# Kernel tuning notes

Measured on AMD Instinct MI355X. Metric: run time of the kernel, lower is better.

The kernel has to match this reference:

```python
import jax, jax.numpy as jnp
import numpy as np

B, L_TOT, C = 64, 8192, 4
WIN = 16
H = 64
NL = 8
GROUPS = 8          # head groups
SA_GROUP = 4        # SortAttn group (hard-coded default)
GH = H * 2 // SA_GROUP   # 32
SEG = 4
CLS = 4
IN_SIZE = C * WIN   # 64 == H (all layers share input dim)


def _shuffle(x):
    # torch Shuffle: transpose(-1,-2).contiguous().view(original_shape)
    return jnp.swapaxes(x, -1, -2).reshape(x.shape)


def setup_inputs() -> dict:
    key = jax.random.key(0)
    ks = jax.random.split(key, 32)
    s = 0.1
    f32 = jnp.float32
    return {
        "x": jax.random.normal(ks[0], (B, L_TOT, C), f32),
        "h0_param": jnp.zeros((NL, 1, H), f32),
        "gru_w_ih": (jax.random.normal(ks[1], (NL, 3 * H, IN_SIZE), f32) * s),
        "gru_w_hh": (jax.random.normal(ks[2], (NL, 3 * H, H), f32) * s),
        "gru_b_ih": (jax.random.normal(ks[3], (NL, 3 * H), f32) * s),
        "gru_b_hh": (jax.random.normal(ks[4], (NL, 3 * H), f32) * s),
        "attn_w1": (jax.random.normal(ks[5], (NL, H, H), f32) * s),
        "attn_w2": (jax.random.normal(ks[6], (NL, GH, GH), f32) * s),
        "attn_w3": (jax.random.normal(ks[7], (NL, GH, GH), f32) * s),
        "attn_w4": (jax.random.normal(ks[8], (NL, H, 2 * H), f32) * s),
        "seg_w1": (jax.random.normal(ks[9], (SEG, H // GROUPS), f32) * s),
        "seg_b1": (jax.random.normal(ks[10], (SEG,), f32) * s),
        "seg_w2": (jax.random.normal(ks[11], (SEG, SEG), f32) * s),
        "seg_b2": (jax.random.normal(ks[12], (SEG,), f32) * s),
        "seg_w3": (jax.random.normal(ks[13], (SEG, SEG), f32) * s),
        "seg_b3": (jax.random.normal(ks[14], (SEG,), f32) * s),
        "seg_w4": (jax.random.normal(ks[15], (WIN, GROUPS), f32) * s),
        "seg_b4": (jax.random.normal(ks[16], (WIN,), f32) * s),
        "cls_w1": (jax.random.normal(ks[17], (CLS, H // GROUPS), f32) * s),
        "cls_b1": (jax.random.normal(ks[18], (CLS,), f32) * s),
        "cls_w2": (jax.random.normal(ks[19], (CLS, CLS), f32) * s),
        "cls_b2": (jax.random.normal(ks[20], (CLS,), f32) * s),
        "cls_w3": (jax.random.normal(ks[21], (CLS, CLS), f32) * s),
        "cls_b3": (jax.random.normal(ks[22], (CLS,), f32) * s),
        "cls_w4": (jax.random.normal(ks[23], (CLS, CLS * GROUPS), f32) * s),
        "cls_b4": (jax.random.normal(ks[24], (CLS,), f32) * s),
    }


def reference(x, h0_param, gru_w_ih, gru_w_hh, gru_b_ih, gru_b_hh,
              attn_w1, attn_w2, attn_w3, attn_w4,
              seg_w1, seg_b1, seg_w2, seg_b2, seg_w3, seg_b3, seg_w4, seg_b4,
              cls_w1, cls_b1, cls_w2, cls_b2, cls_w3, cls_b3, cls_w4, cls_b4):
    b, l, c = x.shape
    lw = l // WIN
    xs = x.reshape(b, lw, WIN * c)                     # (b, lw, IN_SIZE)
    h0 = jnp.broadcast_to(h0_param, (NL, b, H))        # hidden_0 * ones(1,b,1)

    def gru_cell(inp, h, w_ih, w_hh, b_ih, b_hh):
        gi = inp @ w_ih.T + b_ih                       # (b, 3H)
        gh = h @ w_hh.T + b_hh
        i_r, i_z, i_n = jnp.split(gi, 3, axis=1)
        h_r, h_z, h_n = jnp.split(gh, 3, axis=1)
        r = jax.nn.sigmoid(i_r + h_r)
        z = jax.nn.sigmoid(i_z + h_z)
        n = jnp.tanh(i_n + r * h_n)
        return (1.0 - z) * n + z * h

    def sort_attn(h, w1, w2, w3, w4):
        se = jnp.stack([h, jnp.sort(h, axis=1)], axis=1)   # (b, 2, H)
        a = se @ w1.T                                       # (b, 2, H)
        a = a.reshape(b, SA_GROUP, GH)                      # Flatten+Unflatten
        a = _shuffle(a) @ w2.T
        a = jax.nn.relu(_shuffle(a) @ w3.T)
        scores = jax.nn.sigmoid(a.reshape(b, SA_GROUP * GH) @ w4.T)  # (b, H)
        return h * scores

    def step(hidden, xt):
        inp = xt
        new = []
        for i in range(NL):
            hi = gru_cell(inp, hidden[i], gru_w_ih[i], gru_w_hh[i], gru_b_ih[i], gru_b_hh[i])
            hi = sort_attn(hi, attn_w1[i], attn_w2[i], attn_w3[i], attn_w4[i])
            new.append(hi)
            inp = hi
        return jnp.stack(new, axis=0), inp

    h_final, outs = jax.lax.scan(step, h0, jnp.swapaxes(xs, 0, 1))
    ys = jnp.swapaxes(outs, 0, 1)                      # (b, lw, H)

    # ---- seg head ----
    t = ys.reshape(b, lw, GROUPS, H // GROUPS)         # (b, lw, 8, 8)
    t = t @ seg_w1.T + seg_b1                          # (b, lw, 8, 4)
    t = _shuffle(t) @ seg_w2.T + seg_b2
    t = _shuffle(t) @ seg_w3.T + seg_b3
    t = t.reshape(b, lw, SEG, GROUPS)                  # Flatten(2)+Unflatten
    t = t @ seg_w4.T + seg_b4
    seg = jnp.swapaxes(t, -1, -2).reshape(b, lw * WIN, SEG)  # (b, l, 4)

    # ---- avg_pool1d(k=11, s=1) with 10 zero history frames ----
    pool_in = jnp.concatenate([jnp.zeros((b, 10, SEG), seg.dtype), seg], axis=1)
    cs = jnp.concatenate([jnp.zeros((b, 1, SEG), seg.dtype),
                          jnp.cumsum(pool_in, axis=1)], axis=1)
    pool_seg = (cs[:, 11:] - cs[:, :-11]) / 11.0       # (b, l, 4)

    # ---- cls head ----
    u = ys.reshape(b * lw, GROUPS, H // GROUPS)
    u = u @ cls_w1.T + cls_b1
    u = _shuffle(u) @ cls_w2.T + cls_b2
    u = jax.nn.relu(_shuffle(u) @ cls_w3.T + cls_b3)
    cls = u.reshape(b * lw, CLS * GROUPS) @ cls_w4.T + cls_b4
    cls = cls.reshape(b, lw, CLS).mean(axis=1)         # (b, 4)

    return (pool_seg, cls, ys, h_final, seg)
```

## Files before the change

kernel.cpp:

```cpp
#include <hip/hip_runtime.h>
#include <math.h>

#define LW  512

typedef unsigned short u16;
typedef float f32x4 __attribute__((ext_vector_type(4)));
typedef u16 u16x4 __attribute__((ext_vector_type(4)));
typedef u16 u16x8 __attribute__((ext_vector_type(8)));
typedef unsigned u32x2v __attribute__((ext_vector_type(2)));
typedef __bf16 bf16x8 __attribute__((ext_vector_type(8)));

__device__ __forceinline__ u16 f2bf(float f) {
    return __builtin_bit_cast(u16, (__bf16)f);
}
__device__ __forceinline__ float bf2f(u16 h) {
    unsigned u = ((unsigned)h) << 16;
    return __builtin_bit_cast(float, u);
}
__device__ __forceinline__ float sigm(float x) {
    return __builtin_amdgcn_rcpf(1.0f + __expf(-x));
}
__device__ __forceinline__ float tanhfast(float x) {
    return 1.0f - 2.0f * __builtin_amdgcn_rcpf(1.0f + __expf(2.0f * x));
}
__device__ __forceinline__ f32x4 mfma16(u16x8 a, u16x8 b, f32x4 c) {
    return __builtin_amdgcn_mfma_f32_16x16x32_bf16(
        __builtin_bit_cast(bf16x8, a), __builtin_bit_cast(bf16x8, b), c, 0, 0, 0);
}
__device__ __forceinline__ unsigned ld_sys(const unsigned* p) {
    return __hip_atomic_load(p, __ATOMIC_RELAXED, __HIP_MEMORY_SCOPE_SYSTEM);
}
__device__ __forceinline__ void st_sys(unsigned* p, unsigned v) {
    __hip_atomic_store(p, v, __ATOMIC_RELAXED, __HIP_MEMORY_SCOPE_SYSTEM);
}
__device__ __forceinline__ void poll_ge(const unsigned* p, unsigned want) {
    while (ld_sys(p) < want) __builtin_amdgcn_s_sleep(2);
    asm volatile("" ::: "memory");
    __builtin_amdgcn_sched_barrier(0);
}
__device__ __forceinline__ void poll4(const unsigned* p, unsigned want) {
    for (;;) {
        unsigned m0 = ld_sys(p + 0), m1 = ld_sys(p + 1);
        unsigned m2 = ld_sys(p + 2), m3 = ld_sys(p + 3);
        unsigned a = m0 < m1 ? m0 : m1;
        unsigned b = m2 < m3 ? m2 : m3;
        if ((a < b ? a : b) >= want) break;
        __builtin_amdgcn_s_sleep(2);
    }
    asm volatile("" ::: "memory");
    __builtin_amdgcn_sched_barrier(0);
}
__device__ __forceinline__ void bar_lgkm() {
    asm volatile("s_waitcnt lgkmcnt(0)" ::: "memory");
    __builtin_amdgcn_s_barrier();
}

template<int CTRL> __device__ __forceinline__ float dppf(float v) {
    return __builtin_bit_cast(float,
        __builtin_amdgcn_mov_dpp(__builtin_bit_cast(int, v), CTRL, 0xF, 0xF, false));
}
template<int OFF> __device__ __forceinline__ float swzf(float v) {
    return __builtin_bit_cast(float,
        __builtin_amdgcn_ds_swizzle(__builtin_bit_cast(int, v), OFF));
}
template<int J> __device__ __forceinline__ float xch(float v) {
    if constexpr (J == 1)  return dppf<0xB1>(v);
    else if constexpr (J == 2)  return dppf<0x4E>(v);
    else if constexpr (J == 4)  return dppf<0x141>(dppf<0x1B>(v));
    else if constexpr (J == 8)  return dppf<0x140>(dppf<0x141>(v));
    else if constexpr (J == 16) return swzf<0x401F>(v);
    else return __shfl_xor(v, 32);
}
#define STG4(KK, J) { \
    float o0 = xch<J>(v0), o1 = xch<J>(v1), o2 = xch<J>(v2), o3 = xch<J>(v3); \
    bool k = (((ln & KK) == 0) == ((ln & J) == 0)); \
    v0 = k ? fminf(v0, o0) : fmaxf(v0, o0); \
    v1 = k ? fminf(v1, o1) : fmaxf(v1, o1); \
    v2 = k ? fminf(v2, o2) : fmaxf(v2, o2); \
    v3 = k ? fminf(v3, o3) : fmaxf(v3, o3); }

__global__ __launch_bounds__(256) void init_flags(unsigned* f) {
    f[blockIdx.x * 256 + threadIdx.x] = 0u;
}

__global__ __launch_bounds__(128) void prep_A(
    const float* __restrict__ aw1, const float* __restrict__ aw2,
    const float* __restrict__ aw3, u16* __restrict__ Abf)
{
    const int l   = blockIdx.x;
    const int tid = threadIdx.x;
    __shared__ float T1[128][65];
    __shared__ float T2[128][65];
    for (int ch = 0; ch < 2; ++ch) {
        for (int i = tid; i < 128 * 64; i += 128) {
            int f = i >> 6, j = i & 63;
            int s = ch * 64 + j;
            T1[f][j] = ((f >> 6) == (s >> 6))
                       ? aw1[l * 4096 + (f & 63) * 64 + (s & 63)] : 0.f;
        }
        __syncthreads();
        for (int i = tid; i < 128 * 64; i += 128) {
            int gg = i >> 6, j = i & 63;
            int n = gg & 31, r = gg >> 5;
            float acc = 0.f;
            #pragma unroll 8
            for (int k = 0; k < 32; ++k) {
                int g = r * 32 + k;
                int src = (g & 3) * 32 + (g >> 2);
                acc += aw2[l * 1024 + n * 32 + k] * T1[src][j];
            }
            T2[gg][j] = acc;
        }
        __syncthreads();
        for (int i = tid; i < 128 * 64; i += 128) {
            int ff = i >> 6, j = i & 63;
            int n = ff & 31, r = ff >> 5;
            float acc = 0.f;
            #pragma unroll 8
            for (int k = 0; k < 32; ++k) {
                int g = r * 32 + k;
                int src = (g & 3) * 32 + (g >> 2);
                acc += aw3[l * 1024 + n * 32 + k] * T2[src][j];
            }
            Abf[((size_t)l * 128 + ff) * 128 + ch * 64 + j] = f2bf(acc);
        }
        __syncthreads();
    }
}

__global__ __launch_bounds__(256, 1) void rnn_kernel(
    const float* __restrict__ x, const float* __restrict__ h0,
    const float* __restrict__ w_ih, const float* __restrict__ w_hh,
    const float* __restrict__ bih, const float* __restrict__ bhh,
    const u16* __restrict__ Abf, const float* __restrict__ aw4,
    float* __restrict__ ys, float* __restrict__ hfin,
    unsigned* __restrict__ flags, unsigned* __restrict__ ring32, int D)
{
    const int l   = blockIdx.x >> 3;
    const int g   = blockIdx.x & 7;
    const int bb0 = g * 8;
    const int tid = threadIdx.x;
    const int w   = tid >> 6;
    const int ln  = tid & 63;
    const int l15 = ln & 15;
    const int l4  = ln >> 4;
    const bool bp = (D < LW);

    unsigned* myflag = flags + (size_t)(l * 8 + g) * 32;
    unsigned* pflag  = flags + (size_t)((l - 1) * 8 + g) * 32;
    unsigned* myccnt = flags + 4096 + (size_t)(l * 8 + g) * 32;
    unsigned* nccnt  = flags + 4096 + (size_t)((l + 1) * 8 + g) * 32;

    __shared__ __align__(16) u16 Hin[2][16][72];
    __shared__ __align__(16) u16 hbf[16][72];
    __shared__ __align__(16) u16 seF[16][136];
    __shared__ __align__(16) u16 w4A[16][136];

    for (int i = tid; i < 16 * 72; i += 256) {
        int r = i / 72, c = i % 72;
        if (r >= 8) { Hin[0][r][c] = 0; Hin[1][r][c] = 0; hbf[r][c] = 0; }
    }
    for (int i = tid; i < 16 * 136; i += 256) {
        int r = i / 136;
        if (r >= 8) { w4A[r][i % 136] = 0; seF[r][i % 136] = 0; }
    }

    const int o = 16 * w + l15;
    auto ldw8 = [](const float* p) {
        float4 v0 = *(const float4*)p;
        float4 v1 = *(const float4*)(p + 4);
        u16x8 r;
        r[0] = f2bf(v0.x); r[1] = f2bf(v0.y); r[2] = f2bf(v0.z); r[3] = f2bf(v0.w);
        r[4] = f2bf(v1.x); r[5] = f2bf(v1.y); r[6] = f2bf(v1.z); r[7] = f2bf(v1.w);
        return r;
    };
    const float* ih = w_ih + l * 12288;
    const float* hh = w_hh + l * 12288;
    u16x8 Br[4], Bz[4], Bni[2], Bnh[2], B4f[4], BA[2][4];
    Br[0] = ldw8(ih + o * 64 + l4 * 8);        Br[1] = ldw8(ih + o * 64 + 32 + l4 * 8);
    Br[2] = ldw8(hh + o * 64 + l4 * 8);        Br[3] = ldw8(hh + o * 64 + 32 + l4 * 8);
    Bz[0] = ldw8(ih + (64 + o) * 64 + l4 * 8); Bz[1] = ldw8(ih + (64 + o) * 64 + 32 + l4 * 8);
    Bz[2] = ldw8(hh + (64 + o) * 64 + l4 * 8); Bz[3] = ldw8(hh + (64 + o) * 64 + 32 + l4 * 8);
    Bni[0] = ldw8(ih + (128 + o) * 64 + l4 * 8); Bni[1] = ldw8(ih + (128 + o) * 64 + 32 + l4 * 8);
    Bnh[0] = ldw8(hh + (128 + o) * 64 + l4 * 8); Bnh[1] = ldw8(hh + (128 + o) * 64 + 32 + l4 * 8);
    #pragma unroll
    for (int kk = 0; kk < 4; ++kk)
        B4f[kk] = ldw8(aw4 + l * 8192 + o * 128 + kk * 32 + l4 * 8);
    #pragma unroll
    for (int nt = 0; nt < 2; ++nt)
        #pragma unroll
        for (int kk = 0; kk < 4; ++kk)
            BA[nt][kk] = *(const u16x8*)&Abf[((size_t)l * 128 + (16 * (2 * w + nt) + l15)) * 128
                                             + kk * 32 + l4 * 8];

    const float brs  = bih[l * 192 + o]       + bhh[l * 192 + o];
    const float bzs  = bih[l * 192 + 64 + o]  + bhh[l * 192 + 64 + o];
    const float bnis = bih[l * 192 + 128 + o];
    const float bnhs = bhh[l * 192 + 128 + o];

    float hreg[4];
    {
        float hv = h0[l * 64 + o];
        #pragma unroll
        for (int j = 0; j < 4; ++j) hreg[j] = hv;
        if (l4 < 2) {
            u16 hb = f2bf(hv);
            #pragma unroll
            for (int j = 0; j < 4; ++j) hbf[l4 * 4 + j][o] = hb;
        }
    }

    float4 stf = {0.f, 0.f, 0.f, 0.f};
    unsigned st0 = 0, st1 = 0;
    if (w >= 2) {
        const int rr = (tid - 128) >> 4, c4 = ((tid - 128) & 15) * 4;
        if (l == 0) {
            float4 a = *(const float4*)(x + (size_t)(bb0 + rr) * 32768 + c4);
            u16x4 hv;
            hv[0] = f2bf(a.x); hv[1] = f2bf(a.y); hv[2] = f2bf(a.z); hv[3] = f2bf(a.w);
            *(u16x4*)&Hin[0][rr][c4] = hv;
            stf = *(const float4*)(x + (size_t)(bb0 + rr) * 32768 + 64 + c4);
        } else {
            poll4(pflag, 1u);
            const unsigned* sp0 = ring32 + ((size_t)((l - 1) * 8 + g) * D + 0) * 256 + rr * 32 + (c4 >> 1);
            unsigned a0 = ld_sys(sp0), a1 = ld_sys(sp0 + 1);
            u32x2v dv = {a0, a1};
            *(u16x4*)&Hin[0][rr][c4] = __builtin_bit_cast(u16x4, dv);
            poll4(pflag, 2u);
            const unsigned* sp1 = ring32 + ((size_t)((l - 1) * 8 + g) * D + 1) * 256 + rr * 32 + (c4 >> 1);
            st0 = ld_sys(sp1); st1 = ld_sys(sp1 + 1);
        }
    }
    __syncthreads();

    u16x8 pAg0 = *(const u16x8*)&Hin[0][l15][l4 * 8];
    u16x8 pAg1 = *(const u16x8*)&Hin[0][l15][32 + l4 * 8];

    for (int t = 0; t < LW; ++t) {
        float hg[4];
        {
            u16x8 Ah0 = *(const u16x8*)&hbf[l15][l4 * 8];
            u16x8 Ah1 = *(const u16x8*)&hbf[l15][32 + l4 * 8];
            f32x4 z4 = {0.f, 0.f, 0.f, 0.f};
            f32x4 aR = z4, aZ = z4, aNI = z4, aNH = z4;
            aR = mfma16(pAg0, Br[0], aR);  aR = mfma16(pAg1, Br[1], aR);
            aR = mfma16(Ah0, Br[2], aR);   aR = mfma16(Ah1, Br[3], aR);
            aZ = mfma16(pAg0, Bz[0], aZ);  aZ = mfma16(pAg1, Bz[1], aZ);
            aZ = mfma16(Ah0, Bz[2], aZ);   aZ = mfma16(Ah1, Bz[3], aZ);
            aNI = mfma16(pAg0, Bni[0], aNI); aNI = mfma16(pAg1, Bni[1], aNI);
            aNH = mfma16(Ah0, Bnh[0], aNH);  aNH = mfma16(Ah1, Bnh[1], aNH);
            #pragma unroll
            for (int j = 0; j < 4; ++j) {
                float r  = sigm(aR[j] + brs);
                float zz = sigm(aZ[j] + bzs);
                float nn = tanhfast(aNI[j] + bnis + r * (aNH[j] + bnhs));
                hg[j] = (1.0f - zz) * nn + zz * hreg[j];
            }
            if (l4 < 2) {
                #pragma unroll
                for (int j = 0; j < 4; ++j) seF[l4 * 4 + j][o] = f2bf(hg[j]);
            }
        }
        bar_lgkm();

        if (l < 7) {
            asm volatile("s_waitcnt vmcnt(0)" ::: "memory");
            if (ln == 0) st_sys(myflag + w, (unsigned)t);
        }
        if (w < 2) {
            const int r0 = 4 * w;
            float v0 = bf2f(seF[r0 + 0][ln]);
            float v1 = bf2f(seF[r0 + 1][ln]);
            float v2 = bf2f(seF[r0 + 2][ln]);
            float v3 = bf2f(seF[r0 + 3][ln]);
            STG4(2, 1)
            STG4(4, 2)  STG4(4, 1)
            STG4(8, 4)  STG4(8, 2)  STG4(8, 1)
            STG4(16, 8) STG4(16, 4) STG4(16, 2) STG4(16, 1)
            STG4(32, 16) STG4(32, 8) STG4(32, 4) STG4(32, 2) STG4(32, 1)
            STG4(64, 32) STG4(64, 16) STG4(64, 8) STG4(64, 4) STG4(64, 2) STG4(64, 1)
            seF[r0 + 0][64 + ln] = f2bf(v0);
            seF[r0 + 1][64 + ln] = f2bf(v1);
            seF[r0 + 2][64 + ln] = f2bf(v2);
            seF[r0 + 3][64 + ln] = f2bf(v3);
        } else {
            const int rr = (tid - 128) >> 4, c4 = ((tid - 128) & 15) * 4;
            if (t + 1 < LW) {
                u16x4 hv;
                if (l == 0) {
                    hv[0] = f2bf(stf.x); hv[1] = f2bf(stf.y);
                    hv[2] = f2bf(stf.z); hv[3] = f2bf(stf.w);
                } else {
                    u32x2v dv = {st0, st1};
                    hv = __builtin_bit_cast(u16x4, dv);
                }
                *(u16x4*)&Hin[(t + 1) & 1][rr][c4] = hv;
            }
            if (t + 2 < LW) {
                if (l == 0) {
                    stf = *(const float4*)(x + (size_t)(bb0 + rr) * 32768 + (t + 2) * 64 + c4);
                } else {
                    poll4(pflag, (unsigned)(t + 3));
                    const unsigned* sp = ring32
                        + ((size_t)((l - 1) * 8 + g) * D + ((t + 2) & (D - 1))) * 256
                        + rr * 32 + (c4 >> 1);
                    st0 = ld_sys(sp); st1 = ld_sys(sp + 1);
                }
            }
        }
        bar_lgkm();
        if (bp && l > 0 && tid == 0)
            st_sys(myccnt, (unsigned)(t + 2));

        {
            u16x8 As0 = *(const u16x8*)&seF[l15][l4 * 8];
            u16x8 As1 = *(const u16x8*)&seF[l15][32 + l4 * 8];
            u16x8 As2 = *(const u16x8*)&seF[l15][64 + l4 * 8];
            u16x8 As3 = *(const u16x8*)&seF[l15][96 + l4 * 8];
            f32x4 z4 = {0.f, 0.f, 0.f, 0.f};
            f32x4 c0 = z4, c1 = z4;
            c0 = mfma16(As0, BA[0][0], c0); c0 = mfma16(As1, BA[0][1], c0);
            c0 = mfma16(As2, BA[0][2], c0); c0 = mfma16(As3, BA[0][3], c0);
            c1 = mfma16(As0, BA[1][0], c1); c1 = mfma16(As1, BA[1][1], c1);
            c1 = mfma16(As2, BA[1][2], c1); c1 = mfma16(As3, BA[1][3], c1);
            if (l4 < 2) {
                #pragma unroll
                for (int j = 0; j < 4; ++j) {
                    int m = l4 * 4 + j;
                    w4A[m][16 * (2 * w + 0) + l15] = f2bf(fmaxf(c0[j], 0.0f));
                    w4A[m][16 * (2 * w + 1) + l15] = f2bf(fmaxf(c1[j], 0.0f));
                }
            }
        }
        bar_lgkm();

        {
            u16x8 A40 = *(const u16x8*)&w4A[l15][l4 * 8];
            u16x8 A41 = *(const u16x8*)&w4A[l15][32 + l4 * 8];
            u16x8 A42 = *(const u16x8*)&w4A[l15][64 + l4 * 8];
            u16x8 A43 = *(const u16x8*)&w4A[l15][96 + l4 * 8];
            pAg0 = *(const u16x8*)&Hin[(t + 1) & 1][l15][l4 * 8];
            pAg1 = *(const u16x8*)&Hin[(t + 1) & 1][l15][32 + l4 * 8];
            f32x4 cs = {0.f, 0.f, 0.f, 0.f};
            cs = mfma16(A40, B4f[0], cs);
            cs = mfma16(A41, B4f[1], cs);
            cs = mfma16(A42, B4f[2], cs);
            cs = mfma16(A43, B4f[3], cs);

            if (bp && l < 7 && t >= D) {
                poll_ge(nccnt, (unsigned)(t - D + 1));
            }
            unsigned* slotp = ring32 + ((size_t)(l * 8 + g) * D + (t & (D - 1))) * 256;
            float hn[4]; u16 hb[4];
            #pragma unroll
            for (int j = 0; j < 4; ++j) {
                hn[j] = hg[j] * sigm(cs[j]);
                hreg[j] = hn[j];
                hb[j] = f2bf(hn[j]);
            }
            if (l4 < 2) {
                #pragma unroll
                for (int j = 0; j < 4; ++j) {
                    int row = l4 * 4 + j;
                    hbf[row][o] = hb[j];
                    if (l == 7) ys[(((size_t)(bb0 + row) << 9) + t) * 64 + o] = hn[j];
                    if (t == 511) hfin[((l << 6) + bb0 + row) * 64 + o] = hn[j];
                }
            }
            if (l < 7) {
                #pragma unroll
                for (int j = 0; j < 4; ++j) {
                    unsigned ob = (unsigned)__shfl_xor((int)(unsigned)hb[j], 1) & 0xffffu;
                    if (l4 < 2 && !(l15 & 1)) {
                        unsigned word = (unsigned)hb[j] | (ob << 16);
                        st_sys(&slotp[(l4 * 4 + j) * 32 + (o >> 1)], word);
                    }
                }
            }
        }
        bar_lgkm();
    }

    if (l < 7) {
        asm volatile("s_waitcnt vmcnt(0)" ::: "memory");
        if (ln == 0) st_sys(myflag + w, 512u);
    }
}

__global__ __launch_bounds__(256) void heads_kernel(
    const float* __restrict__ ys,
    const float* __restrict__ sw1, const float* __restrict__ sb1,
    const float* __restrict__ sw2, const float* __restrict__ sb2,
    const float* __restrict__ sw3, const float* __restrict__ sb3,
    const float* __restrict__ sw4, const float* __restrict__ sb4,
    const float* __restrict__ cw1, const float* __restrict__ cb1,
    const float* __restrict__ cw2, const float* __restrict__ cb2,
    const float* __restrict__ cw3, const float* __restrict__ cb3,
    const float* __restrict__ cw4, const float* __restrict__ cb4,
    float* __restrict__ seg_out, float* __restrict__ cls_tmp)
{
    const int idx = blockIdx.x * 256 + threadIdx.x;
    if (idx >= 64 * LW) return;
    const int b = idx >> 9, t = idx & 511;

    float y[64];
    const float4* yp = (const float4*)(ys + (size_t)idx * 64);
    #pragma unroll
    for (int i = 0; i < 16; ++i) {
        float4 v = yp[i];
        y[4 * i + 0] = v.x; y[4 * i + 1] = v.y; y[4 * i + 2] = v.z; y[4 * i + 3] = v.w;
    }

    float t1[8][4], t2[8][4], t3[8][4];

    #pragma unroll
    for (int g = 0; g < 8; ++g)
        #pragma unroll
        for (int s = 0; s < 4; ++s) {
            float acc = sb1[s];
            #pragma unroll
            for (int k = 0; k < 8; ++k) acc = fmaf(y[g * 8 + k], sw1[s * 8 + k], acc);
            t1[g][s] = acc;
        }
    #pragma unroll
    for (int i = 0; i < 8; ++i) {
        float sh[4];
        #pragma unroll
        for (int j = 0; j < 4; ++j) { int m = i * 4 + j; sh[j] = t1[m & 7][m >> 3]; }
        #pragma unroll
        for (int s = 0; s < 4; ++s) {
            float acc = sb2[s];
            #pragma unroll
            for (int j = 0; j < 4; ++j) acc = fmaf(sh[j], sw2[s * 4 + j], acc);
            t2[i][s] = acc;
        }
    }
    #pragma unroll
    for (int i = 0; i < 8; ++i) {
        float sh[4];
        #pragma unroll
        for (int j = 0; j < 4; ++j) { int m = i * 4 + j; sh[j] = t2[m & 7][m >> 3]; }
        #pragma unroll
        for (int s = 0; s < 4; ++s) {
            float acc = sb3[s];
            #pragma unroll
            for (int j = 0; j < 4; ++j) acc = fmaf(sh[j], sw3[s * 4 + j], acc);
            t3[i][s] = acc;
        }
    }
    #pragma unroll
    for (int w = 0; w < 16; ++w) {
        float o4[4];
        #pragma unroll
        for (int s = 0; s < 4; ++s) {
            float acc = sb4[w];
            #pragma unroll
            for (int j = 0; j < 8; ++j) {
                int f = s * 8 + j;
                acc = fmaf(t3[f >> 2][f & 3], sw4[w * 8 + j], acc);
            }
            o4[s] = acc;
        }
        float4 vv = {o4[0], o4[1], o4[2], o4[3]};
        ((float4*)seg_out)[b * 8192 + t * 16 + w] = vv;
    }

    #pragma unroll
    for (int g = 0; g < 8; ++g)
        #pragma unroll
        for (int s = 0; s < 4; ++s) {
            float acc = cb1[s];
            #pragma unroll
            for (int k = 0; k < 8; ++k) acc = fmaf(y[g * 8 + k], cw1[s * 8 + k], acc);
            t1[g][s] = acc;
        }
    #pragma unroll
    for (int i = 0; i < 8; ++i) {
        float sh[4];
        #pragma unroll
        for (int j = 0; j < 4; ++j) { int m = i * 4 + j; sh[j] = t1[m & 7][m >> 3]; }
        #pragma unroll
        for (int s = 0; s < 4; ++s) {
            float acc = cb2[s];
            #pragma unroll
            for (int j = 0; j < 4; ++j) acc = fmaf(sh[j], cw2[s * 4 + j], acc);
            t2[i][s] = acc;
        }
    }
    #pragma unroll
    for (int i = 0; i < 8; ++i) {
        float sh[4];
        #pragma unroll
        for (int j = 0; j < 4; ++j) { int m = i * 4 + j; sh[j] = t2[m & 7][m >> 3]; }
        #pragma unroll
        for (int s = 0; s < 4; ++s) {
            float acc = cb3[s];
            #pragma unroll
            for (int j = 0; j < 4; ++j) acc = fmaf(sh[j], cw3[s * 4 + j], acc);
            t3[i][s] = fmaxf(acc, 0.f);
        }
    }
    float cc[4];
    #pragma unroll
    for (int c = 0; c < 4; ++c) {
        float acc = cb4[c];
        #pragma unroll
        for (int k = 0; k < 32; ++k)
            acc = fmaf(t3[k >> 2][k & 3], cw4[c * 32 + k], acc);
        cc[c] = acc;
    }
    float4 cv = {cc[0], cc[1], cc[2], cc[3]};
    ((float4*)cls_tmp)[idx] = cv;
}

__global__ __launch_bounds__(256) void cls_reduce_kernel(
    const float* __restrict__ cls_tmp, float* __restrict__ cls_out)
{
    const int tid = threadIdx.x;
    const int b = tid >> 2, q = tid & 3;
    float ax = 0.f, ay = 0.f, az = 0.f, aw = 0.f;
    for (int t = q; t < 512; t += 4) {
        float4 v = ((const float4*)cls_tmp)[b * 512 + t];
        ax += v.x; ay += v.y; az += v.z; aw += v.w;
    }
    ax += __shfl_xor(ax, 1); ay += __shfl_xor(ay, 1);
    az += __shfl_xor(az, 1); aw += __shfl_xor(aw, 1);
    ax += __shfl_xor(ax, 2); ay += __shfl_xor(ay, 2);
    az += __shfl_xor(az, 2); aw += __shfl_xor(aw, 2);
    if (q == 0) {
        float4 rv = {ax / 512.f, ay / 512.f, az / 512.f, aw / 512.f};
        ((float4*)cls_out)[b] = rv;
    }
}

__global__ __launch_bounds__(256) void pool_kernel(
    const float* __restrict__ seg, float* __restrict__ pool_out)
{
    const int idx = blockIdx.x * 256 + threadIdx.x;
    if (idx >= 64 * 8192) return;
    const int b = idx >> 13, ll = idx & 8191;
    float ax = 0.f, ay = 0.f, az = 0.f, aw = 0.f;
    int j0 = ll - 10; if (j0 < 0) j0 = 0;
    for (int j = j0; j <= ll; ++j) {
        float4 v = ((const float4*)seg)[b * 8192 + j];
        ax += v.x; ay += v.y; az += v.z; aw += v.w;
    }
    const float inv = 1.0f / 11.0f;
    float4 ov = {ax * inv, ay * inv, az * inv, aw * inv};
    ((float4*)pool_out)[idx] = ov;
}

extern "C" void kernel_launch(void* const* d_in, const int* in_sizes, int n_in,
                              void* d_out, int out_size, void* d_ws, size_t ws_size,
                              hipStream_t stream)
{
    const float* x    = (const float*)d_in[0];
    const float* h0   = (const float*)d_in[1];
    const float* w_ih = (const float*)d_in[2];
    const float* w_hh = (const float*)d_in[3];
    const float* bihp = (const float*)d_in[4];
    const float* bhhp = (const float*)d_in[5];
    const float* aw1  = (const float*)d_in[6];
    const float* aw2  = (const float*)d_in[7];
    const float* aw3  = (const float*)d_in[8];
    const float* aw4  = (const float*)d_in[9];
    const float* sw1  = (const float*)d_in[10];
    const float* sb1  = (const float*)d_in[11];
    const float* sw2  = (const float*)d_in[12];
    const float* sb2  = (const float*)d_in[13];
    const float* sw3  = (const float*)d_in[14];
    const float* sb3  = (const float*)d_in[15];
    const float* sw4  = (const float*)d_in[16];
    const float* sb4  = (const float*)d_in[17];
    const float* cw1  = (const float*)d_in[18];
    const float* cb1  = (const float*)d_in[19];
    const float* cw2  = (const float*)d_in[20];
    const float* cb2  = (const float*)d_in[21];
    const float* cw3  = (const float*)d_in[22];
    const float* cb3  = (const float*)d_in[23];
    const float* cw4  = (const float*)d_in[24];
    const float* cb4  = (const float*)d_in[25];

    float* out      = (float*)d_out;
    float* pool_out = out;
    float* cls_out  = out + 2097152;
    float* ys_out   = out + 2097408;
    float* hfin     = out + 4194560;
    float* seg_out  = out + 4227328;
    float* cls_tmp  = pool_out;

    unsigned* flags  = (unsigned*)d_ws;
    u16*      Abf    = (u16*)((char*)d_ws + 32768);
    unsigned* ring32 = (unsigned*)((char*)d_ws + 32768 + 262144);

    size_t hdr = 32768 + 262144;
    size_t slots = (ws_size > hdr) ? (ws_size - hdr) / (56ull * 256 * 4) : 8;
    int D = 512;
    if (slots < 512) {
        D = 8;
        while ((size_t)(D * 2) <= slots && D < 512) D <<= 1;
    }

    init_flags<<<32, 256, 0, stream>>>(flags);
    prep_A<<<8, 128, 0, stream>>>(aw1, aw2, aw3, Abf);
    rnn_kernel<<<64, 256, 0, stream>>>(x, h0, w_ih, w_hh, bihp, bhhp,
                                       Abf, aw4, ys_out, hfin,
                                       flags, ring32, D);
    heads_kernel<<<128, 256, 0, stream>>>(ys_out, sw1, sb1, sw2, sb2, sw3, sb3, sw4, sb4,
                                          cw1, cb1, cw2, cb2, cw3, cb3, cw4, cb4,
                                          seg_out, cls_tmp);
    cls_reduce_kernel<<<1, 256, 0, stream>>>(cls_tmp, cls_out);
    pool_kernel<<<2048, 256, 0, stream>>>(seg_out, pool_out);
}
```

Baseline: 1.378 ms.

## Spread sort across all four waves and overlap input staging with MFMA

The bitonic sort of the eight 64-element rows was done by two waves handling four rows each while the other two waves staged the next input. Now all four waves each sort two rows, and the Hin staging, cross-layer poll and prefetch move after the MFMA issue of the next phase, so they overlap with matrix work. This shortens the critical path of the serial per-timestep sort. The trade-off is that the poll and load latency now sits inside the MFMA phase and can delay the barrier that follows.

Result: slower. 1.480 ms (+7.4%).

```diff
diff --git a/kernel.cpp b/kernel.cpp
--- a/kernel.cpp
+++ b/kernel.cpp
@@ -71,13 +71,11 @@
     else if constexpr (J == 16) return swzf<0x401F>(v);
     else return __shfl_xor(v, 32);
 }
-#define STG4(KK, J) { \
-    float o0 = xch<J>(v0), o1 = xch<J>(v1), o2 = xch<J>(v2), o3 = xch<J>(v3); \
-    bool k = (((ln & KK) == 0) == ((ln & J) == 0)); \
+#define STG2(KK, J) { \
+    float o0 = xch<J>(v0), o1 = xch<J>(v1); \
+    bool k = (((ln & KK) == 0) == (((ln) & J) == 0)); \
     v0 = k ? fminf(v0, o0) : fmaxf(v0, o0); \
-    v1 = k ? fminf(v1, o1) : fmaxf(v1, o1); \
-    v2 = k ? fminf(v2, o2) : fmaxf(v2, o2); \
-    v3 = k ? fminf(v3, o3) : fmaxf(v3, o3); }
+    v1 = k ? fminf(v1, o1) : fmaxf(v1, o1); }
 
 __global__ __launch_bounds__(256) void init_flags(unsigned* f) {
     f[blockIdx.x * 256 + threadIdx.x] = 0u;
@@ -267,46 +265,17 @@
             asm volatile("s_waitcnt vmcnt(0)" ::: "memory");
             if (ln == 0) st_sys(myflag + w, (unsigned)t);
         }
-        if (w < 2) {
-            const int r0 = 4 * w;
-            float v0 = bf2f(seF[r0 + 0][ln]);
-            float v1 = bf2f(seF[r0 + 1][ln]);
-            float v2 = bf2f(seF[r0 + 2][ln]);
-            float v3 = bf2f(seF[r0 + 3][ln]);
-            STG4(2, 1)
-            STG4(4, 2)  STG4(4, 1)
-            STG4(8, 4)  STG4(8, 2)  STG4(8, 1)
-            STG4(16, 8) STG4(16, 4) STG4(16, 2) STG4(16, 1)
-            STG4(32, 16) STG4(32, 8) STG4(32, 4) STG4(32, 2) STG4(32, 1)
-            STG4(64, 32) STG4(64, 16) STG4(64, 8) STG4(64, 4) STG4(64, 2) STG4(64, 1)
-            seF[r0 + 0][64 + ln] = f2bf(v0);
-            seF[r0 + 1][64 + ln] = f2bf(v1);
-            seF[r0 + 2][64 + ln] = f2bf(v2);
-            seF[r0 + 3][64 + ln] = f2bf(v3);
-        } else {
-            const int rr = (tid - 128) >> 4, c4 = ((tid - 128) & 15) * 4;
-            if (t + 1 < LW) {
-                u16x4 hv;
-                if (l == 0) {
-                    hv[0] = f2bf(stf.x); hv[1] = f2bf(stf.y);
-                    hv[2] = f2bf(stf.z); hv[3] = f2bf(stf.w);
-                } else {
-                    u32x2v dv = {st0, st1};
-                    hv = __builtin_bit_cast(u16x4, dv);
-                }
-                *(u16x4*)&Hin[(t + 1) & 1][rr][c4] = hv;
-            }
-            if (t + 2 < LW) {
-                if (l == 0) {
-                    stf = *(const float4*)(x + (size_t)(bb0 + rr) * 32768 + (t + 2) * 64 + c4);
-                } else {
-                    poll4(pflag, (unsigned)(t + 3));
-                    const unsigned* sp = ring32
-                        + ((size_t)((l - 1) * 8 + g) * D + ((t + 2) & (D - 1))) * 256
-                        + rr * 32 + (c4 >> 1);
-                    st0 = ld_sys(sp); st1 = ld_sys(sp + 1);
-                }
-            }
+        {
+            float v0 = bf2f(seF[2 * w][ln]);
+            float v1 = bf2f(seF[2 * w + 1][ln]);
+            STG2(2, 1)
+            STG2(4, 2)  STG2(4, 1)
+            STG2(8, 4)  STG2(8, 2)  STG2(8, 1)
+            STG2(16, 8) STG2(16, 4) STG2(16, 2) STG2(16, 1)
+            STG2(32, 16) STG2(32, 8) STG2(32, 4) STG2(32, 2) STG2(32, 1)
+            STG2(64, 32) STG2(64, 16) STG2(64, 8) STG2(64, 4) STG2(64, 2) STG2(64, 1)
+            seF[2 * w][64 + ln]     = f2bf(v0);
+            seF[2 * w + 1][64 + ln] = f2bf(v1);
         }
         bar_lgkm();
         if (bp && l > 0 && tid == 0)
@@ -323,6 +292,31 @@
             c0 = mfma16(As2, BA[0][2], c0); c0 = mfma16(As3, BA[0][3], c0);
             c1 = mfma16(As0, BA[1][0], c1); c1 = mfma16(As1, BA[1][1], c1);
             c1 = mfma16(As2, BA[1][2], c1); c1 = mfma16(As3, BA[1][3], c1);
+            if (w >= 2) {
+                const int rr = (tid - 128) >> 4, c4 = ((tid - 128) & 15) * 4;
+                if (t + 1 < LW) {
+                    u16x4 hv;
+                    if (l == 0) {
+                        hv[0] = f2bf(stf.x); hv[1] = f2bf(stf.y);
+                        hv[2] = f2bf(stf.z); hv[3] = f2bf(stf.w);
+                    } else {
+                        u32x2v dv = {st0, st1};
+                        hv = __builtin_bit_cast(u16x4, dv);
+                    }
+                    *(u16x4*)&Hin[(t + 1) & 1][rr][c4] = hv;
+                }
+                if (t + 2 < LW) {
+                    if (l == 0) {
+                        stf = *(const float4*)(x + (size_t)(bb0 + rr) * 32768 + (t + 2) * 64 + c4);
+                    } else {
+                        poll4(pflag, (unsigned)(t + 3));
+                        const unsigned* sp = ring32
+                            + ((size_t)((l - 1) * 8 + g) * D + ((t + 2) & (D - 1))) * 256
+                            + rr * 32 + (c4 >> 1);
+                        st0 = ld_sys(sp); st1 = ld_sys(sp + 1);
+                    }
+                }
+            }
             if (l4 < 2) {
                 #pragma unroll
                 for (int j = 0; j < 4; ++j) {
```
